# Kernel tuning notes

Hardware: AMD Instinct MI355X
Metric: run time of the kernel (lower is better)

The kernel has to match this reference:

```python
import jax, jax.numpy as jnp
import numpy as np
import math

B, S, D_MODEL, H = 128, 256, 128, 8
D_K = D_MODEL // H
FACTOR = 5
SAMPLE_K = FACTOR * int(math.ceil(math.log(S)))   # 30 sampled keys per query
N_TOP = min(FACTOR * int(math.ceil(math.log(S))), S)  # 30 active queries
KSIZE = 7


def setup_inputs() -> dict:
    key = jax.random.key(0)
    ks = jax.random.split(key, 10)
    s = 0.05
    return {
        "query": jax.random.normal(ks[0], (B, S, D_MODEL), jnp.float32),
        "key": jax.random.normal(ks[1], (B, S, D_MODEL), jnp.float32),
        "value": jax.random.normal(ks[2], (B, S, D_MODEL), jnp.float32),
        "conv_k_w": jax.random.normal(ks[3], (S, S, KSIZE), jnp.float32) * s,
        "conv_k_b": jax.random.normal(ks[4], (S,), jnp.float32) * s,
        "conv_v_w": jax.random.normal(ks[5], (S, S, KSIZE), jnp.float32) * s,
        "conv_v_b": jax.random.normal(ks[6], (S,), jnp.float32) * s,
        "lin_w": jax.random.normal(ks[7], (D_MODEL, D_MODEL), jnp.float32) * s,
        "lin_b": jax.random.normal(ks[8], (D_MODEL,), jnp.float32) * s,
        "index_sample": jax.random.randint(ks[9], (S, SAMPLE_K), 0, S),
    }


def _rotary(x):
    # x: [B,S,D]; complex rotation of consecutive pairs, angle = pos * theta^{-2i/D}
    half = D_MODEL // 2
    freqs = 1.0 / (10000.0 ** (jnp.arange(0, D_MODEL, 2, dtype=jnp.float32) / D_MODEL))
    ang = jnp.arange(S, dtype=jnp.float32)[:, None] * freqs[None, :]  # [S, half]
    cos, sin = jnp.cos(ang), jnp.sin(ang)
    xr = x.reshape(B, S, half, 2)
    out_r = xr[..., 0] * cos - xr[..., 1] * sin
    out_i = xr[..., 0] * sin + xr[..., 1] * cos
    return jnp.stack([out_r, out_i], axis=-1).reshape(B, S, D_MODEL)


def _causal_conv(x, w, b):
    # x: [B, C=S, L=D_MODEL]; causal => left-pad (KSIZE-1). w: [C_out, C_in, K]
    y = jax.lax.conv_general_dilated(
        x, w, window_strides=(1,), padding=[(KSIZE - 1, 0)],
        dimension_numbers=("NCH", "OIH", "NCH"))
    return y + b[None, :, None]


def reference(query, key, value, conv_k_w, conv_k_b, conv_v_w, conv_v_b,
              lin_w, lin_b, index_sample):
    q, k = _rotary(query), _rotary(key)
    k = _causal_conv(k, conv_k_w, conv_k_b)        # conv over seq-as-channels
    v = _causal_conv(value, conv_v_w, conv_v_b)
    # [B,S,D] -> [B,H,S,Dk]
    q = q.reshape(B, S, H, D_K).transpose(0, 2, 1, 3)
    k = k.reshape(B, S, H, D_K).transpose(0, 2, 1, 3)
    v = v.reshape(B, S, H, D_K).transpose(0, 2, 1, 3)

    # --- ProbSparse attention (Informer), mask=None ---
    k_sample = k[:, :, index_sample, :]                       # [B,H,S,SAMPLE_K,Dk]
    qk_sample = jnp.einsum('bhld,bhlsd->bhls', q, k_sample)   # sampled scores
    M = qk_sample.max(axis=-1) - qk_sample.mean(axis=-1)      # sparsity measure [B,H,S]
    _, m_top = jax.lax.top_k(M, N_TOP)                        # active queries [B,H,u]
    q_reduce = jnp.take_along_axis(q, m_top[..., None], axis=2)  # [B,H,u,Dk]
    scores = jnp.einsum('bhud,bhld->bhul', q_reduce, k) / jnp.sqrt(jnp.float32(D_K))
    attn = jax.nn.softmax(scores, axis=-1)
    out_top = jnp.einsum('bhul,bhld->bhud', attn, v)          # [B,H,u,Dk]
    # initial context = mean of V (no mask); overwrite rows of active queries
    context = jnp.broadcast_to(v.mean(axis=2, keepdims=True), (B, H, S, D_K))
    bi = jnp.arange(B)[:, None, None]
    hi = jnp.arange(H)[None, :, None]
    context = context.at[bi, hi, m_top].set(out_top)

    x = context.transpose(0, 2, 1, 3).reshape(B, S, D_MODEL)
    return x @ lin_w.T + lin_b
```

## Files before the change

### kernel.cpp

```cpp
#include <hip/hip_runtime.h>
#include <math.h>

constexpr int B_  = 128;
constexpr int S_  = 256;
constexpr int D_  = 128;
constexpr int H_  = 8;
constexpr int DK_ = 16;
constexpr int SK_ = 30;
constexpr int NT_ = 30;

typedef short short8  __attribute__((ext_vector_type(8)));
typedef float floatx4 __attribute__((ext_vector_type(4)));

__device__ inline ushort bf16_rne(float f) {
    unsigned u = __float_as_uint(f);
    u += 0x7fffu + ((u >> 16) & 1u);
    return (ushort)(u >> 16);
}
__device__ inline float bf16_to_f(ushort h) {
    return __uint_as_float(((unsigned)h) << 16);
}

__global__ __launch_bounds__(256) void wprep_kernel(
    const float* __restrict__ wk, const float* __restrict__ wv,
    const float* __restrict__ lw,
    ushort* __restrict__ wk_hi, ushort* __restrict__ wk_lo,
    ushort* __restrict__ wv_hi,
    ushort* __restrict__ lw_hi, ushort* __restrict__ lw_lo,
    float* __restrict__ trig)
{
    int tid = blockIdx.x * 256 + threadIdx.x;
    if (tid < 458752) {
        int t  = tid >> 16;
        int oi = tid & 65535;
        float fk = wk[(size_t)oi * 7 + t];
        ushort hk = bf16_rne(fk);
        wk_hi[tid] = hk;
        wk_lo[tid] = bf16_rne(fk - bf16_to_f(hk));
        wv_hi[tid] = bf16_rne(wv[(size_t)oi * 7 + t]);
    } else if (tid < 475136) {
        int ec = tid - 458752;
        float f = lw[ec];
        ushort hi = bf16_rne(f);
        lw_hi[ec] = hi;
        lw_lo[ec] = bf16_rne(f - bf16_to_f(hi));
    } else {
        int t2 = tid - 475136;
        int f = t2 & 63, l = t2 >> 6;
        double freq = exp(((double)(-f) / 64.0) * 9.210340371976184);
        double ang  = (double)l * freq;
        trig[t2 * 2]     = (float)cos(ang);
        trig[t2 * 2 + 1] = (float)sin(ang);
    }
}

__global__ __launch_bounds__(256) void rotcvt_kernel(
    const float* __restrict__ q, const float* __restrict__ k,
    const float* __restrict__ value, const float* __restrict__ trig,
    float* __restrict__ q_h,
    ushort* __restrict__ khi_t, ushort* __restrict__ klo_t,
    ushort* __restrict__ vhi_t)
{
    __shared__ float tile[64 * 132];
    int b  = blockIdx.x;
    int lc = blockIdx.y;
    int ph = blockIdx.z;
    int tid = threadIdx.x;

    if (ph == 0) {
        for (int s = tid; s < 2048; s += 256) {
            int l = s >> 5, c4 = s & 31;
            int lg = lc * 64 + l;
            float4 qv = *(const float4*)(q + (((size_t)b * 256) + lg) * 128 + c4 * 4);
            float4 tg = *(const float4*)(trig + ((size_t)lg * 64 + 2 * c4) * 2);
            float r0 = qv.x * tg.x - qv.y * tg.y;
            float i0 = qv.x * tg.y + qv.y * tg.x;
            float r1 = qv.z * tg.z - qv.w * tg.w;
            float i1 = qv.z * tg.w + qv.w * tg.z;
            int h = c4 >> 2, dk = (c4 & 3) * 4;
            *(float4*)(q_h + (((size_t)b * 8 + h) * 256 + lg) * 16 + dk) =
                make_float4(r0, i0, r1, i1);
        }
        return;
    }

    if (ph == 1) {
        for (int s = tid; s < 2048; s += 256) {
            int l = s >> 5, c4 = s & 31;
            int lg = lc * 64 + l;
            float4 kv = *(const float4*)(k + (((size_t)b * 256) + lg) * 128 + c4 * 4);
            float4 tg = *(const float4*)(trig + ((size_t)lg * 64 + 2 * c4) * 2);
            float r0 = kv.x * tg.x - kv.y * tg.y;
            float i0 = kv.x * tg.y + kv.y * tg.x;
            float r1 = kv.z * tg.z - kv.w * tg.w;
            float i1 = kv.z * tg.w + kv.w * tg.z;
            *(float4*)(tile + l * 132 + c4 * 4) = make_float4(r0, i0, r1, i1);
        }
        __syncthreads();
        int d = tid >> 1, half = tid & 1;
        alignas(16) ushort hh[32], ll[32];
#pragma unroll
        for (int j = 0; j < 32; j++) {
            float f = tile[(half * 32 + j) * 132 + d];
            ushort hb = bf16_rne(f);
            hh[j] = hb;
            ll[j] = bf16_rne(f - bf16_to_f(hb));
        }
        size_t off = (((size_t)b * 128) + d) * 256 + lc * 64 + half * 32;
#pragma unroll
        for (int m = 0; m < 4; m++) ((uint4*)(khi_t + off))[m] = ((uint4*)hh)[m];
#pragma unroll
        for (int m = 0; m < 4; m++) ((uint4*)(klo_t + off))[m] = ((uint4*)ll)[m];
        return;
    }

    for (int s = tid; s < 2048; s += 256) {
        int l = s >> 5, c4 = s & 31;
        *(float4*)(tile + l * 132 + c4 * 4) =
            *(const float4*)(value + (((size_t)b * 256) + lc * 64 + l) * 128 + c4 * 4);
    }
    __syncthreads();
    {
        int d = tid >> 1, half = tid & 1;
        alignas(16) ushort hh[32];
#pragma unroll
        for (int j = 0; j < 32; j++)
            hh[j] = bf16_rne(tile[(half * 32 + j) * 132 + d]);
        size_t off = (((size_t)b * 128) + d) * 256 + lc * 64 + half * 32;
#pragma unroll
        for (int m = 0; m < 4; m++) ((uint4*)(vhi_t + off))[m] = ((uint4*)hh)[m];
    }
}

__global__ __launch_bounds__(256, 2) void conv5_kernel(
    const ushort* __restrict__ khi_t, const ushort* __restrict__ klo_t,
    const ushort* __restrict__ vhi_t,
    const ushort* __restrict__ wk_hi, const ushort* __restrict__ wk_lo,
    const ushort* __restrict__ wv_hi,
    const float* __restrict__ kbias, const float* __restrict__ vbias,
    float* __restrict__ k_h, float* __restrict__ v_h)
{
    constexpr int LI = 72;
    __shared__ ushort xhi[70 * LI];
    __shared__ ushort xlo[70 * LI];

    const bool kp = (blockIdx.z == 0);
    const ushort* xg   = kp ? khi_t : vhi_t;
    const ushort* whi  = kp ? wk_hi : wv_hi;
    const float*  bias = kp ? kbias : vbias;
    float* yh          = kp ? k_h : v_h;

    int b    = blockIdx.x;
    int dblk = blockIdx.y;
    int tid  = threadIdx.x;
    int lane = tid & 63, wid = tid >> 6;
    int lm = lane & 15, kb = lane >> 4;
    int obase = wid * 64;

    floatx4 acc[16];
#pragma unroll
    for (int i = 0; i < 16; i++) acc[i] = (floatx4){0.f, 0.f, 0.f, 0.f};

    const short8 zero8 = {0, 0, 0, 0, 0, 0, 0, 0};

    for (int ic = 0; ic < 4; ic++) {
        __syncthreads();
        for (int s = tid; s < 560; s += 256) {
            int r = s >> 3, p = s & 7;
            int gd = dblk * 64 - 6 + r;
            size_t g = (((size_t)b * 128) + gd) * 256 + ic * 64 + p * 8;
            short8 vh = (gd >= 0) ? *(const short8*)(xg + g) : zero8;
            *(short8*)(xhi + r * LI + p * 8) = vh;
            if (kp) {
                short8 vl = (gd >= 0) ? *(const short8*)(klo_t + g) : zero8;
                *(short8*)(xlo + r * LI + p * 8) = vl;
            }
        }
        __syncthreads();
#pragma unroll
        for (int ks = 0; ks < 2; ks++) {
            int ibase = ic * 64 + ks * 32 + kb * 8;
#pragma unroll
            for (int t = 0; t < 7; t++) {
                short8 xh[4], xl[4];
#pragma unroll
                for (int nd = 0; nd < 4; nd++) {
                    int arow = (nd * 16 + lm + t) * LI + ks * 32 + kb * 8;
                    xh[nd] = *(const short8*)(xhi + arow);
                    if (kp) xl[nd] = *(const short8*)(xlo + arow);
                }
                short8 wh[4], wl[4];
#pragma unroll
                for (int po = 0; po < 4; po++) {
                    size_t woff = (size_t)t * 65536
                                + (size_t)(obase + po * 16 + lm) * 256 + ibase;
                    wh[po] = *(const short8*)(whi + woff);
                    if (kp) wl[po] = *(const short8*)(wk_lo + woff);
                }
#pragma unroll
                for (int po = 0; po < 4; po++) {
#pragma unroll
                    for (int nd = 0; nd < 4; nd++) {
                        int a = po * 4 + nd;
                        acc[a] = __builtin_amdgcn_mfma_f32_16x16x32_bf16(xh[nd], wh[po], acc[a], 0, 0, 0);
                        if (kp) {
                            acc[a] = __builtin_amdgcn_mfma_f32_16x16x32_bf16(xl[nd], wh[po], acc[a], 0, 0, 0);
                            acc[a] = __builtin_amdgcn_mfma_f32_16x16x32_bf16(xh[nd], wl[po], acc[a], 0, 0, 0);
                        }
                    }
                }
            }
        }
    }

#pragma unroll
    for (int po = 0; po < 4; po++) {
        int o = obase + po * 16 + lm;
        float bv = bias[o];
#pragma unroll
        for (int nd = 0; nd < 4; nd++) {
            int dhi = dblk * 4 + nd;
#pragma unroll
            for (int r = 0; r < 4; r++) {
                int dk = kb * 4 + r;
                yh[(((size_t)b * 8 + dhi) * 256 + o) * 16 + dk] = acc[po * 4 + nd][r] + bv;
            }
        }
    }
}

__global__ __launch_bounds__(256) void topk_attn_kernel(
    const float* __restrict__ q_h, const float* __restrict__ k_h,
    const float* __restrict__ v_h, const int* __restrict__ idxs,
    ushort* __restrict__ ctx_hi, ushort* __restrict__ ctx_lo)
{
    __shared__ float ks[S_ * 20];
    __shared__ float vs[S_ * 20];
    __shared__ float Marr[S_];
    __shared__ float qs[NT_][16];
    __shared__ float partial[16][17];
    __shared__ float vmean_s[16];
    __shared__ int sel_s[NT_];
    __shared__ int selflag[S_];
    __shared__ int cnt;

    int bh = blockIdx.x, b = bh >> 3, h = bh & 7;
    int tid = threadIdx.x;
    if (tid == 0) cnt = 0;
    selflag[tid] = 0;

    const float* kp = k_h + (size_t)bh * S_ * DK_;
    const float* vp = v_h + (size_t)bh * S_ * DK_;
    for (int idx = tid; idx < S_ * DK_; idx += 256) {
        int r = idx >> 4, c = idx & 15;
        ks[r * 20 + c] = kp[idx];
        vs[r * 20 + c] = vp[idx];
    }

    float qr[16];
    const float4* qp = (const float4*)(q_h + ((size_t)bh * S_ + tid) * DK_);
#pragma unroll
    for (int i = 0; i < 4; i++) {
        float4 t4 = qp[i];
        qr[4*i] = t4.x; qr[4*i+1] = t4.y; qr[4*i+2] = t4.z; qr[4*i+3] = t4.w;
    }
    int idxr[SK_];
    const int* ip = idxs + tid * SK_;
#pragma unroll
    for (int s = 0; s < SK_; s++) idxr[s] = ip[s];
    __syncthreads();

    float mx = -1e30f, sm = 0.f;
#pragma unroll
    for (int s = 0; s < SK_; s++) {
        const float4* kr = (const float4*)(ks + idxr[s] * 20);
        float4 k0 = kr[0], k1 = kr[1], k2 = kr[2], k3 = kr[3];
        float d0 = qr[0]*k0.x, d1 = qr[1]*k0.y, d2 = qr[2]*k0.z, d3 = qr[3]*k0.w;
        d0 = fmaf(qr[4],  k1.x, d0); d1 = fmaf(qr[5],  k1.y, d1);
        d2 = fmaf(qr[6],  k1.z, d2); d3 = fmaf(qr[7],  k1.w, d3);
        d0 = fmaf(qr[8],  k2.x, d0); d1 = fmaf(qr[9],  k2.y, d1);
        d2 = fmaf(qr[10], k2.z, d2); d3 = fmaf(qr[11], k2.w, d3);
        d0 = fmaf(qr[12], k3.x, d0); d1 = fmaf(qr[13], k3.y, d1);
        d2 = fmaf(qr[14], k3.z, d2); d3 = fmaf(qr[15], k3.w, d3);
        float dot = (d0 + d1) + (d2 + d3);
        mx = fmaxf(mx, dot);
        sm += dot;
    }
    Marr[tid] = mx - sm * (1.0f / 30.0f);

    {
        int dk = tid & 15, chunk = tid >> 4;
        float s = 0.f;
#pragma unroll
        for (int r = 0; r < 16; r++) s += vs[(chunk * 16 + r) * 20 + dk];
        partial[chunk][dk] = s;
    }
    __syncthreads();

    if (tid < 16) {
        float s = 0.f;
#pragma unroll
        for (int c = 0; c < 16; c++) s += partial[c][tid];
        vmean_s[tid] = s * (1.0f / 256.0f);
    }
    {
        float M = Marr[tid];
        int higher = 0;
        for (int j = 0; j < S_; j++) {
            float Mj = Marr[j];
            if (Mj > M || (Mj == M && j < tid)) higher++;
        }
        if (higher < NT_) {
            int slot = atomicAdd(&cnt, 1);
            sel_s[slot] = tid;
            selflag[tid] = 1;
        }
    }
    __syncthreads();

    for (int idx = tid; idx < NT_ * 16; idx += 256) {
        int u = idx >> 4, c = idx & 15;
        qs[u][c] = q_h[((size_t)bh * S_ + sel_s[u]) * DK_ + c];
    }
    __syncthreads();

    if (!selflag[tid]) {
        alignas(16) ushort hh[16], ll[16];
#pragma unroll
        for (int i = 0; i < 16; i++) {
            float v = vmean_s[i];
            ushort hb = bf16_rne(v);
            hh[i] = hb;
            ll[i] = bf16_rne(v - bf16_to_f(hb));
        }
        size_t off = ((size_t)(b * S_ + tid)) * D_ + h * DK_;
        ((uint4*)(ctx_hi + off))[0] = ((uint4*)hh)[0];
        ((uint4*)(ctx_hi + off))[1] = ((uint4*)hh)[1];
        ((uint4*)(ctx_lo + off))[0] = ((uint4*)ll)[0];
        ((uint4*)(ctx_lo + off))[1] = ((uint4*)ll)[1];
    }

    int g = tid >> 3, j = tid & 7;
    if (g < NT_) {
        float qreg[16];
        const float4* q4 = (const float4*)qs[g];
#pragma unroll
        for (int i = 0; i < 4; i++) {
            float4 t4 = q4[i];
            qreg[4*i] = t4.x; qreg[4*i+1] = t4.y; qreg[4*i+2] = t4.z; qreg[4*i+3] = t4.w;
        }
        float e[32];
        float mxs = -1e30f;
#pragma unroll
        for (int li = 0; li < 32; li++) {
            int l = j + li * 8;
            const float4* kr = (const float4*)(ks + l * 20);
            float4 k0 = kr[0], k1 = kr[1], k2 = kr[2], k3 = kr[3];
            float d0 = qreg[0]*k0.x, d1 = qreg[1]*k0.y, d2 = qreg[2]*k0.z, d3 = qreg[3]*k0.w;
            d0 = fmaf(qreg[4],  k1.x, d0); d1 = fmaf(qreg[5],  k1.y, d1);
            d2 = fmaf(qreg[6],  k1.z, d2); d3 = fmaf(qreg[7],  k1.w, d3);
            d0 = fmaf(qreg[8],  k2.x, d0); d1 = fmaf(qreg[9],  k2.y, d1);
            d2 = fmaf(qreg[10], k2.z, d2); d3 = fmaf(qreg[11], k2.w, d3);
            d0 = fmaf(qreg[12], k3.x, d0); d1 = fmaf(qreg[13], k3.y, d1);
            d2 = fmaf(qreg[14], k3.z, d2); d3 = fmaf(qreg[15], k3.w, d3);
            e[li] = ((d0 + d1) + (d2 + d3)) * 0.25f;
            mxs = fmaxf(mxs, e[li]);
        }
        mxs = fmaxf(mxs, __shfl_xor(mxs, 1));
        mxs = fmaxf(mxs, __shfl_xor(mxs, 2));
        mxs = fmaxf(mxs, __shfl_xor(mxs, 4));
        float se = 0.f;
#pragma unroll
        for (int li = 0; li < 32; li++) {
            e[li] = __expf(e[li] - mxs);
            se += e[li];
        }
        se += __shfl_xor(se, 1);
        se += __shfl_xor(se, 2);
        se += __shfl_xor(se, 4);
        float inv = 1.0f / se;

        int dk0 = j * 2;
        int gbase = tid & 56;
        float o0 = 0.f, o1 = 0.f;
        for (int li = 0; li < 32; li++) {
#pragma unroll
            for (int m = 0; m < 8; m++) {
                float p = __shfl(e[li], gbase | m);
                float2 vv = *(const float2*)(vs + (li * 8 + m) * 20 + dk0);
                o0 = fmaf(p, vv.x, o0);
                o1 = fmaf(p, vv.y, o1);
            }
        }
        int lrow = sel_s[g];
        float v0 = o0 * inv, v1 = o1 * inv;
        ushort h0 = bf16_rne(v0), h1 = bf16_rne(v1);
        ushort l0 = bf16_rne(v0 - bf16_to_f(h0));
        ushort l1 = bf16_rne(v1 - bf16_to_f(h1));
        size_t off = ((size_t)(b * S_ + lrow)) * D_ + h * DK_ + dk0;
        *(uint*)(ctx_hi + off) = (uint)h0 | ((uint)h1 << 16);
        *(uint*)(ctx_lo + off) = (uint)l0 | ((uint)l1 << 16);
    }
}

__global__ __launch_bounds__(256) void linear_mfma_kernel(
    const ushort* __restrict__ ctx_hi, const ushort* __restrict__ ctx_lo,
    const ushort* __restrict__ w_hi, const ushort* __restrict__ w_lo,
    const float* __restrict__ bias, float* __restrict__ out)
{
    __shared__ ushort ahi[64 * 136];
    __shared__ ushort alo[64 * 136];

    int tid  = threadIdx.x;
    int lane = tid & 63, wid = tid >> 6;
    int lm = lane & 15, kb = lane >> 4;
    size_t rowbase = (size_t)blockIdx.x * 64;

    for (int idx = tid; idx < 1024; idx += 256) {
        int row = idx >> 4, c16 = idx & 15;
        short8 vh = *(const short8*)(ctx_hi + (rowbase + row) * 128 + c16 * 8);
        short8 vl = *(const short8*)(ctx_lo + (rowbase + row) * 128 + c16 * 8);
        *(short8*)(ahi + row * 136 + c16 * 8) = vh;
        *(short8*)(alo + row * 136 + c16 * 8) = vl;
    }
    __syncthreads();

    floatx4 acc[8];
#pragma unroll
    for (int i = 0; i < 8; i++) acc[i] = (floatx4){0.f, 0.f, 0.f, 0.f};

    const ushort* arow_h = ahi + (wid * 16 + lm) * 136 + kb * 8;
    const ushort* arow_l = alo + (wid * 16 + lm) * 136 + kb * 8;

#pragma unroll
    for (int kstep = 0; kstep < 4; kstep++) {
        short8 afh = *(const short8*)(arow_h + kstep * 32);
        short8 afl = *(const short8*)(arow_l + kstep * 32);
        short8 bfh[8], bfl[8];
#pragma unroll
        for (int nf = 0; nf < 8; nf++) {
            bfh[nf] = *(const short8*)(w_hi + (size_t)(nf * 16 + lm) * 128 + kstep * 32 + kb * 8);
            bfl[nf] = *(const short8*)(w_lo + (size_t)(nf * 16 + lm) * 128 + kstep * 32 + kb * 8);
        }
#pragma unroll
        for (int nf = 0; nf < 8; nf++) {
            acc[nf] = __builtin_amdgcn_mfma_f32_16x16x32_bf16(afh, bfh[nf], acc[nf], 0, 0, 0);
            acc[nf] = __builtin_amdgcn_mfma_f32_16x16x32_bf16(afl, bfh[nf], acc[nf], 0, 0, 0);
            acc[nf] = __builtin_amdgcn_mfma_f32_16x16x32_bf16(afh, bfl[nf], acc[nf], 0, 0, 0);
        }
    }

#pragma unroll
    for (int nf = 0; nf < 8; nf++) {
        int col = nf * 16 + lm;
        float bv = bias[col];
#pragma unroll
        for (int r = 0; r < 4; r++) {
            int row = wid * 16 + kb * 4 + r;
            out[(rowbase + row) * 128 + col] = acc[nf][r] + bv;
        }
    }
}

extern "C" void kernel_launch(void* const* d_in, const int* in_sizes, int n_in,
                              void* d_out, int out_size, void* d_ws, size_t ws_size,
                              hipStream_t stream)
{
    const float* query = (const float*)d_in[0];
    const float* key   = (const float*)d_in[1];
    const float* value = (const float*)d_in[2];
    const float* ckw   = (const float*)d_in[3];
    const float* ckb   = (const float*)d_in[4];
    const float* cvw   = (const float*)d_in[5];
    const float* cvb   = (const float*)d_in[6];
    const float* lw    = (const float*)d_in[7];
    const float* lb    = (const float*)d_in[8];
    const int*   isamp = (const int*)d_in[9];
    float* out = (float*)d_out;
    float* ws  = (float*)d_ws;

    const size_t NBSD = (size_t)B_ * S_ * D_;
    float* q_h  = ws;
    float* kbuf = ws + NBSD;
    float* k_h  = ws + 2 * NBSD;
    float* v_h  = ws + 3 * NBSD;
    int*   sel  = (int*)(ws + 4 * NBSD);
    ushort* wk_hi = (ushort*)(sel + B_ * H_ * NT_);
    ushort* wk_lo = wk_hi + 7 * 65536;
    ushort* wv_hi = wk_lo + 7 * 65536;
    ushort* lw_hi = wv_hi + 7 * 65536;
    ushort* lw_lo = lw_hi + 16384;
    float*  trig  = (float*)(lw_lo + 16384);
    ushort* khi_t = (ushort*)(trig + 32768);
    ushort* klo_t = khi_t + NBSD;
    ushort* vhi_t = klo_t + NBSD;
    ushort* ctx_hi = (ushort*)kbuf;
    ushort* ctx_lo = ctx_hi + NBSD;

    wprep_kernel<<<dim3(1920), 256, 0, stream>>>(ckw, cvw, lw, wk_hi, wk_lo,
                                                 wv_hi, lw_hi, lw_lo, trig);
    rotcvt_kernel<<<dim3(B_, 4, 3), 256, 0, stream>>>(query, key, value, trig,
                                                      q_h, khi_t, klo_t, vhi_t);
    conv5_kernel<<<dim3(B_, 2, 2), 256, 0, stream>>>(khi_t, klo_t, vhi_t,
                                                     wk_hi, wk_lo, wv_hi,
                                                     ckb, cvb, k_h, v_h);
    topk_attn_kernel<<<dim3(B_ * H_), 256, 0, stream>>>(q_h, k_h, v_h, isamp,
                                                        ctx_hi, ctx_lo);
    linear_mfma_kernel<<<dim3(512), 256, 0, stream>>>(ctx_hi, ctx_lo, lw_hi,
                                                      lw_lo, lb, out);
}
```

Baseline: 279.9 us.

## Software-pipeline conv kernel: prefetch next input stage and weight/A fragments into registers

```diff
diff --git a/kernel.cpp b/kernel.cpp
--- a/kernel.cpp
+++ b/kernel.cpp
@@ -132,7 +132,7 @@
     }
 }
 
-__global__ __launch_bounds__(256, 2) void conv5_kernel(
+__global__ __launch_bounds__(256, 2) void conv6_kernel(
     const ushort* __restrict__ khi_t, const ushort* __restrict__ klo_t,
     const ushort* __restrict__ vhi_t,
     const ushort* __restrict__ wk_hi, const ushort* __restrict__ wk_lo,
@@ -163,52 +163,89 @@
 
     const short8 zero8 = {0, 0, 0, 0, 0, 0, 0, 0};
 
+    short8 sh[3], sl[3];
+    auto load_stage = [&](int ic) {
+#pragma unroll
+        for (int it = 0; it < 3; it++) {
+            int s = tid + it * 256;
+            int r = s >> 3, p = s & 7;
+            int gd = dblk * 64 - 6 + r;
+            bool ok = (s < 560) && (gd >= 0);
+            size_t g = (((size_t)b * 128) + gd) * 256 + ic * 64 + p * 8;
+            sh[it] = ok ? *(const short8*)(xg + g) : zero8;
+            if (kp) sl[it] = ok ? *(const short8*)(klo_t + g) : zero8;
+        }
+    };
+    auto store_stage = [&]() {
+#pragma unroll
+        for (int it = 0; it < 3; it++) {
+            int s = tid + it * 256;
+            if (s < 560) {
+                int r = s >> 3, p = s & 7;
+                *(short8*)(xhi + r * LI + p * 8) = sh[it];
+                if (kp) *(short8*)(xlo + r * LI + p * 8) = sl[it];
+            }
+        }
+    };
+    auto load_w = [&](int ic, int ks, int t, short8* wh, short8* wl) {
+        int ibase = ic * 64 + ks * 32 + kb * 8;
+#pragma unroll
+        for (int po = 0; po < 4; po++) {
+            size_t woff = (size_t)t * 65536
+                        + (size_t)(obase + po * 16 + lm) * 256 + ibase;
+            wh[po] = *(const short8*)(whi + woff);
+            if (kp) wl[po] = *(const short8*)(wk_lo + woff);
+        }
+    };
+    auto load_a = [&](int ks, int t, short8* xh, short8* xl) {
+#pragma unroll
+        for (int nd = 0; nd < 4; nd++) {
+            int arow = (nd * 16 + lm + t) * LI + ks * 32 + kb * 8;
+            xh[nd] = *(const short8*)(xhi + arow);
+            if (kp) xl[nd] = *(const short8*)(xlo + arow);
+        }
+    };
+
+    short8 whc[4], wlc[4], whn[4], wln[4];
+    short8 xhc[4], xlc[4], xhn[4], xln[4];
+
+    load_stage(0);
+    load_w(0, 0, 0, whc, wlc);
+
+#pragma unroll 1
     for (int ic = 0; ic < 4; ic++) {
         __syncthreads();
-        for (int s = tid; s < 560; s += 256) {
-            int r = s >> 3, p = s & 7;
-            int gd = dblk * 64 - 6 + r;
-            size_t g = (((size_t)b * 128) + gd) * 256 + ic * 64 + p * 8;
-            short8 vh = (gd >= 0) ? *(const short8*)(xg + g) : zero8;
-            *(short8*)(xhi + r * LI + p * 8) = vh;
-            if (kp) {
-                short8 vl = (gd >= 0) ? *(const short8*)(klo_t + g) : zero8;
-                *(short8*)(xlo + r * LI + p * 8) = vl;
+        store_stage();
+        __syncthreads();
+        if (ic < 3) load_stage(ic + 1);
+        load_a(0, 0, xhc, xlc);
+#pragma unroll
+        for (int step = 0; step < 14; step++) {
+            int ks = step / 7, t = step % 7;
+            (void)ks; (void)t;
+            if (step < 13) {
+                int ns = step + 1;
+                load_w(ic, ns / 7, ns % 7, whn, wln);
+                load_a(ns / 7, ns % 7, xhn, xln);
+            } else if (ic < 3) {
+                load_w(ic + 1, 0, 0, whn, wln);
             }
-        }
-        __syncthreads();
-#pragma unroll
-        for (int ks = 0; ks < 2; ks++) {
-            int ibase = ic * 64 + ks * 32 + kb * 8;
-#pragma unroll
-            for (int t = 0; t < 7; t++) {
-                short8 xh[4], xl[4];
+#pragma unroll
+            for (int po = 0; po < 4; po++) {
 #pragma unroll
                 for (int nd = 0; nd < 4; nd++) {
-                    int arow = (nd * 16 + lm + t) * LI + ks * 32 + kb * 8;
-                    xh[nd] = *(const short8*)(xhi + arow);
-                    if (kp) xl[nd] = *(const short8*)(xlo + arow);
-                }
-                short8 wh[4], wl[4];
-#pragma unroll
-                for (int po = 0; po < 4; po++) {
-                    size_t woff = (size_t)t * 65536
-                                + (size_t)(obase + po * 16 + lm) * 256 + ibase;
-                    wh[po] = *(const short8*)(whi + woff);
-                    if (kp) wl[po] = *(const short8*)(wk_lo + woff);
-                }
-#pragma unroll
-                for (int po = 0; po < 4; po++) {
-#pragma unroll
-                    for (int nd = 0; nd < 4; nd++) {
-                        int a = po * 4 + nd;
-                        acc[a] = __builtin_amdgcn_mfma_f32_16x16x32_bf16(xh[nd], wh[po], acc[a], 0, 0, 0);
-                        if (kp) {
-                            acc[a] = __builtin_amdgcn_mfma_f32_16x16x32_bf16(xl[nd], wh[po], acc[a], 0, 0, 0);
-                            acc[a] = __builtin_amdgcn_mfma_f32_16x16x32_bf16(xh[nd], wl[po], acc[a], 0, 0, 0);
-                        }
+                    int a = po * 4 + nd;
+                    acc[a] = __builtin_amdgcn_mfma_f32_16x16x32_bf16(xhc[nd], whc[po], acc[a], 0, 0, 0);
+                    if (kp) {
+                        acc[a] = __builtin_amdgcn_mfma_f32_16x16x32_bf16(xlc[nd], whc[po], acc[a], 0, 0, 0);
+                        acc[a] = __builtin_amdgcn_mfma_f32_16x16x32_bf16(xhc[nd], wlc[po], acc[a], 0, 0, 0);
                     }
                 }
+            }
+#pragma unroll
+            for (int i2 = 0; i2 < 4; i2++) {
+                whc[i2] = whn[i2]; wlc[i2] = wln[i2];
+                xhc[i2] = xhn[i2]; xlc[i2] = xln[i2];
             }
         }
     }
@@ -501,7 +538,7 @@
                                                  wv_hi, lw_hi, lw_lo, trig);
     rotcvt_kernel<<<dim3(B_, 4, 3), 256, 0, stream>>>(query, key, value, trig,
                                                       q_h, khi_t, klo_t, vhi_t);
-    conv5_kernel<<<dim3(B_, 2, 2), 256, 0, stream>>>(khi_t, klo_t, vhi_t,
+    conv6_kernel<<<dim3(B_, 2, 2), 256, 0, stream>>>(khi_t, klo_t, vhi_t,
                                                      wk_hi, wk_lo, wv_hi,
                                                      ckb, cvb, k_h, v_h);
     topk_attn_kernel<<<dim3(B_ * H_), 256, 0, stream>>>(q_h, k_h, v_h, isamp,
```

Measured after the change: 308.2 us. 10.1% more time.
